# Kernel optimization log

Hardware: AMD Instinct MI355X
Metric: run time of the kernel (lower is better)

## Reference

```python
import jax, jax.numpy as jnp
import numpy as np
from jax import lax

EPS = 1e-12

def _l2norm(x):
    # F.normalize(x, dim=-1): x / max(||x||, eps)
    n = jnp.sqrt(jnp.sum(x * x, axis=-1, keepdims=True))
    return x / jnp.maximum(n, EPS)

def _knn_edges(z, k):
    """k nearest neighbors (excluding self) via squared euclidean distance.
    Squared distance preserves the top-k ordering of torch.cdist."""
    N = z.shape[0]
    sq = jnp.sum(z * z, axis=1)                        # [N]
    d2 = sq[:, None] + sq[None, :] - 2.0 * (z @ z.T)   # [N, N]
    _, idx = lax.top_k(-d2, k + 1)                     # nearest first; col 0 is self
    tgt = idx[:, 1:].reshape(-1)                       # [N*k]
    src = jnp.repeat(jnp.arange(N, dtype=idx.dtype), k)
    return src, tgt

def _count_components(A):
    """Connected components on dense boolean adjacency A [N,N] via
    min-label propagation with pointer jumping (jit-friendly BFS replacement)."""
    N = A.shape[0]
    labels0 = jnp.arange(N, dtype=jnp.int32)

    def cond(state):
        return state[1]

    def body(state):
        labels, _ = state
        # min label over neighbors (N as sentinel where no edge)
        nbr_min = jnp.min(jnp.where(A, labels[None, :], jnp.int32(N)), axis=1)
        new = jnp.minimum(labels, nbr_min)
        new = new[new]  # pointer jumping: label of my label
        return new, jnp.any(new != labels)

    labels, _ = lax.while_loop(cond, body, (labels0, jnp.array(True)))
    # a node whose final label equals its own index is the component minimum
    return jnp.sum(labels == jnp.arange(N, dtype=jnp.int32))

def _level(feats, W, ratio):
    N = feats.shape[0]
    z = _l2norm(feats @ W.T)                 # Linear(bias=False) then normalize
    k = max(3, int(ratio * N))               # static python int
    k = min(k, N - 1)
    src, tgt = _knn_edges(z, k)
    A = jnp.zeros((N, N), dtype=bool)
    A = A.at[src, tgt].set(True).at[tgt, src].set(True)   # symmetrize
    comps = _count_components(lax.stop_gradient(A))
    num_edges = N * k                                     # src.numel() in torch code
    b0 = comps
    b1 = jnp.maximum(0, num_edges - N + comps)
    return b0, b1

RATIOS = (0.1, 0.05)

def setup_inputs() -> dict:
    key = jax.random.key(0)
    k1, k2, k3 = jax.random.split(key, 3)
    N, C = 4096, 512
    feats = jax.random.normal(k1, (N, C), dtype=jnp.float32)
    W0 = jax.random.normal(k2, (512, C), dtype=jnp.float32) / np.sqrt(C)
    W1 = jax.random.normal(k3, (256, C), dtype=jnp.float32) / np.sqrt(C)
    return {"feats": feats, "W0": W0, "W1": W1}

def reference(feats, W0, W1):
    b0_0, b1_0 = _level(feats, W0, RATIOS[0])
    b0_1, b1_1 = _level(feats, W1, RATIOS[1])
    return jnp.stack([b0_0 + b0_1, b1_0 + b1_1]).astype(jnp.float32)
```

## Files before the change

### kernel.cpp

```cpp
#include <hip/hip_runtime.h>
#include <hip/hip_bf16.h>

#define NPTS   4096
#define ADJ_W  128

typedef __attribute__((ext_vector_type(8))) short short8;
typedef __attribute__((ext_vector_type(8))) unsigned short u16x8;
typedef __attribute__((ext_vector_type(4))) unsigned short u16x4;
typedef __attribute__((ext_vector_type(16))) unsigned char u8x16;
typedef __attribute__((ext_vector_type(4))) float f32x4;
typedef __attribute__((ext_vector_type(4))) int i32x4;
typedef __attribute__((ext_vector_type(4))) unsigned u32x4;

__device__ __forceinline__ unsigned short bf16_bits(float x) {
  __hip_bfloat16 h = __float2bfloat16(x);
  return __builtin_bit_cast(unsigned short, h);
}

__device__ __forceinline__ unsigned char quant8(float f) {
  return (unsigned char)(int)fminf(fmaxf((f + 0.25f) * 512.0f, 0.0f), 255.0f);
}

__device__ __forceinline__ void async16(const void* g, void* l) {
  __builtin_amdgcn_global_load_lds(
      (const __attribute__((address_space(1))) void*)g,
      (__attribute__((address_space(3))) void*)l, 16, 0, 0);
}

__global__ __launch_bounds__(256) void convert_all(
    const float* __restrict__ feats, const float* __restrict__ W0,
    const float* __restrict__ W1, unsigned short* __restrict__ fh,
    unsigned short* __restrict__ wcat) {
  const int NF = 4096 * 512 / 4, NW0 = 512 * 512 / 4, NW1 = 256 * 512 / 4;
  for (int u = blockIdx.x * 256 + threadIdx.x; u < NF + NW0 + NW1;
       u += gridDim.x * 256) {
    const float* src;
    unsigned short* dst;
    int idx;
    if (u < NF)            { src = feats; dst = fh;   idx = u; }
    else if (u < NF + NW0) { src = W0;    dst = wcat; idx = u - NF; }
    else                   { src = W1;    dst = wcat + NW0 * 4; idx = u - NF - NW0; }
    f32x4 v = *(const f32x4*)(src + (size_t)idx * 4);
    u16x4 o;
    #pragma unroll
    for (int e = 0; e < 4; e++) o[e] = bf16_bits(v[e]);
    *(u16x4*)(dst + (size_t)idx * 4) = o;
  }
}

__global__ __launch_bounds__(256) void gemm_bt_f32(
    const __hip_bfloat16* __restrict__ A, const __hip_bfloat16* __restrict__ B,
    float* __restrict__ C, int M, int N, int K) {
  __shared__ __attribute__((aligned(16))) __hip_bfloat16 As[2][128 * 32];
  __shared__ __attribute__((aligned(16))) __hip_bfloat16 Bs[2][128 * 32];
  int tid = threadIdx.x;
  int lane = tid & 63, wave = tid >> 6;
  int wr = wave >> 1, wc = wave & 1;
  int row0 = blockIdx.y * 128, col0 = blockIdx.x * 128;

  f32x4 acc[4][4] = {};
  int r = lane & 15, kh = lane >> 4;

  auto stage = [&](int buf, int k0) {
    #pragma unroll
    for (int q = 0; q < 2; q++) {
      int chunk = q * 256 + tid;
      int row = chunk >> 2;
      int cb = chunk & 3;
      async16(&A[(size_t)(row0 + row) * K + k0 + cb * 8],
              &As[buf][(q * 256 + wave * 64) * 8]);
      async16(&B[(size_t)(col0 + row) * K + k0 + cb * 8],
              &Bs[buf][(q * 256 + wave * 64) * 8]);
    }
  };

  int nt = K >> 5;
  stage(0, 0);
  int cur = 0;
  for (int t = 0; t < nt; t++) {
    if (t + 1 < nt) {
      stage(cur ^ 1, (t + 1) * 32);
      asm volatile("s_waitcnt vmcnt(4)" ::: "memory");
    } else {
      asm volatile("s_waitcnt vmcnt(0)" ::: "memory");
    }
    __builtin_amdgcn_s_barrier();
    __builtin_amdgcn_sched_barrier(0);

    short8 a[4], b[4];
    #pragma unroll
    for (int mi = 0; mi < 4; mi++)
      a[mi] = *(short8*)(&As[cur][(wr * 64 + mi * 16 + r) * 32 + kh * 8]);
    #pragma unroll
    for (int ni = 0; ni < 4; ni++)
      b[ni] = *(short8*)(&Bs[cur][(wc * 64 + ni * 16 + r) * 32 + kh * 8]);
    #pragma unroll
    for (int mi = 0; mi < 4; mi++)
      #pragma unroll
      for (int ni = 0; ni < 4; ni++)
        acc[mi][ni] = __builtin_amdgcn_mfma_f32_16x16x32_bf16(a[mi], b[ni], acc[mi][ni], 0, 0, 0);
    __builtin_amdgcn_s_barrier();
    cur ^= 1;
  }

  int rq = lane >> 4;
  #pragma unroll
  for (int mi = 0; mi < 4; mi++)
    #pragma unroll
    for (int ni = 0; ni < 4; ni++)
      #pragma unroll
      for (int j = 0; j < 4; j++) {
        int rr = row0 + wr * 64 + mi * 16 + rq * 4 + j;
        int cc = col0 + wc * 64 + ni * 16 + r;
        C[(size_t)rr * N + cc] = acc[mi][ni][j];
      }
}

__global__ __launch_bounds__(512) void gemm_s_tri(
    const __hip_bfloat16* __restrict__ Z0, const __hip_bfloat16* __restrict__ Z1,
    unsigned char* __restrict__ S0, unsigned char* __restrict__ S1) {
  __shared__ __attribute__((aligned(16))) __hip_bfloat16 As[3][128 * 32];
  __shared__ __attribute__((aligned(16))) __hip_bfloat16 Bs[3][128 * 32];
  unsigned char* Cs = (unsigned char*)As;

  int b = blockIdx.x;
  int s = (b & 7) * 132 + (b >> 3);
  int lvl = s & 1;
  int t = s >> 1;
  int I = (int)((sqrtf(8.0f * (float)t + 1.0f) - 1.0f) * 0.5f);
  if (t - I * (I + 1) / 2 > I) I++;
  int J = t - I * (I + 1) / 2;

  const __hip_bfloat16* Z = lvl ? Z1 : Z0;
  unsigned char* S = lvl ? S1 : S0;
  int K = lvl ? 256 : 512;
  int row0 = I * 128, col0 = J * 128;

  int tid = threadIdx.x;
  int lane = tid & 63, wave = tid >> 6;
  int wr = wave >> 2, wc = wave & 3;

  f32x4 acc[4][2] = {};
  int r = lane & 15, kh = lane >> 4, rq = lane >> 4;

  auto stage = [&](int buf, int k0) {
    int row = tid >> 2;
    int cb = tid & 3;
    async16(&Z[(size_t)(row0 + row) * K + k0 + cb * 8],
            &As[buf][(wave * 64) * 8]);
    async16(&Z[(size_t)(col0 + row) * K + k0 + cb * 8],
            &Bs[buf][(wave * 64) * 8]);
  };

  int nt = K >> 5;
  stage(0, 0);
  stage(1, 32);
  for (int tt = 0; tt < nt; tt++) {
    int cur = tt % 3;
    if (tt + 2 < nt) stage((tt + 2) % 3, (tt + 2) * 32);
    if (tt + 3 <= nt) {
      asm volatile("s_waitcnt vmcnt(4)" ::: "memory");
    } else if (tt + 2 == nt) {
      asm volatile("s_waitcnt vmcnt(2)" ::: "memory");
    } else {
      asm volatile("s_waitcnt vmcnt(0)" ::: "memory");
    }
    __builtin_amdgcn_s_barrier();
    __builtin_amdgcn_sched_barrier(0);

    short8 a[4], bfr[2];
    #pragma unroll
    for (int mi = 0; mi < 4; mi++)
      a[mi] = *(short8*)(&As[cur][(wr * 64 + mi * 16 + r) * 32 + kh * 8]);
    #pragma unroll
    for (int ni = 0; ni < 2; ni++)
      bfr[ni] = *(short8*)(&Bs[cur][(wc * 32 + ni * 16 + r) * 32 + kh * 8]);
    #pragma unroll
    for (int mi = 0; mi < 4; mi++)
      #pragma unroll
      for (int ni = 0; ni < 2; ni++)
        acc[mi][ni] = __builtin_amdgcn_mfma_f32_16x16x32_bf16(a[mi], bfr[ni], acc[mi][ni], 0, 0, 0);
    __builtin_amdgcn_s_barrier();
  }
  __syncthreads();

  int erow = tid >> 4;
  int ecol = (tid & 15) * 8;

  #pragma unroll
  for (int s4 = 0; s4 < 4; s4++) {
    if (wr == (s4 >> 1)) {
      const int half = s4 & 1;
      #pragma unroll
      for (int mi_l = 0; mi_l < 2; mi_l++) {
        const int mi = half * 2 + mi_l;
        #pragma unroll
        for (int ni = 0; ni < 2; ni++) {
          int lrow0 = mi * 16 + rq * 4 - half * 32;
          int cc = wc * 32 + ni * 16 + r;
          #pragma unroll
          for (int j = 0; j < 4; j++)
            Cs[(lrow0 + j) * 144 + cc] = quant8(acc[mi][ni][j]);
        }
      }
    }
    __syncthreads();
    {
      unsigned long long v = *(const unsigned long long*)(&Cs[erow * 144 + ecol]);
      *(unsigned long long*)(&S[(size_t)(row0 + s4 * 32 + erow) * NPTS + col0 + ecol]) = v;
    }
    __syncthreads();
  }

  if (I != J) {
    #pragma unroll
    for (int s4 = 0; s4 < 4; s4++) {
      if (wc == s4) {
        #pragma unroll
        for (int ni = 0; ni < 2; ni++) {
          int lrow = ni * 16 + r;
          #pragma unroll
          for (int mi = 0; mi < 4; mi++) {
            int rr = wr * 64 + mi * 16 + rq * 4;
            unsigned v = (unsigned)quant8(acc[mi][ni][0])
                       | ((unsigned)quant8(acc[mi][ni][1]) << 8)
                       | ((unsigned)quant8(acc[mi][ni][2]) << 16)
                       | ((unsigned)quant8(acc[mi][ni][3]) << 24);
            *(unsigned*)(&Cs[lrow * 144 + rr]) = v;
          }
        }
      }
      __syncthreads();
      {
        unsigned long long v = *(const unsigned long long*)(&Cs[erow * 144 + ecol]);
        *(unsigned long long*)(&S[(size_t)(col0 + s4 * 32 + erow) * NPTS + row0 + ecol]) = v;
      }
      __syncthreads();
    }
  }
}

__global__ __launch_bounds__(64) void l2norm_fused(const float* __restrict__ Zcat,
                                                   unsigned short* __restrict__ Z0h,
                                                   unsigned short* __restrict__ Z1h) {
  int bid = blockIdx.x;
  int lvl = bid >> 12, row = bid & 4095;
  int D = lvl ? 256 : 512;
  const float* src = Zcat + (size_t)row * 768 + (lvl ? 512 : 0);
  unsigned short* dst = lvl ? (Z1h + (size_t)row * 256) : (Z0h + (size_t)row * 512);
  int d4 = D >> 2;
  int lane = threadIdx.x;
  float ss = 0.f;
  for (int j = lane; j < d4; j += 64) {
    f32x4 v = *(const f32x4*)(src + j * 4);
    ss += v[0] * v[0] + v[1] * v[1] + v[2] * v[2] + v[3] * v[3];
  }
  #pragma unroll
  for (int off = 32; off; off >>= 1) ss += __shfl_xor(ss, off);
  float inv = 1.0f / fmaxf(sqrtf(ss), 1e-12f);
  for (int j = lane; j < d4; j += 64) {
    f32x4 v = *(const f32x4*)(src + j * 4);
    u16x4 o;
    #pragma unroll
    for (int e = 0; e < 4; e++) o[e] = bf16_bits(v[e] * inv);
    *(u16x4*)(dst + j * 4) = o;
  }
}

__global__ __launch_bounds__(256) void select_mark_f(
    const unsigned char* __restrict__ S0, const unsigned char* __restrict__ S1,
    unsigned* __restrict__ adjR) {
  __shared__ int hist[4][256];
  __shared__ int sfx[257];
  __shared__ int wtot[4];
  __shared__ unsigned rowbits[ADJ_W];
  __shared__ int sh_b;
  int bid = blockIdx.x;
  int lvl = bid >> 12, i = bid & 4095;
  int k = lvl ? 204 : 409;
  const unsigned char* row = (lvl ? S1 : S0) + (size_t)i * NPTS;
  unsigned* adj = adjR + ((size_t)lvl * NPTS + i) * ADJ_W;
  int tid = threadIdx.x;
  int lane = tid & 63, wid = tid >> 6;
  int target = k + 1;

  #pragma unroll
  for (int w = 0; w < 4; w++) hist[w][tid] = 0;
  if (tid < ADJ_W) rowbits[tid] = 0;
  __syncthreads();

  u8x16 v = *(const u8x16*)(row + tid * 16);
  #pragma unroll
  for (int e = 0; e < 16; e++)
    atomicAdd(&hist[wid][v[e]], 1);
  __syncthreads();

  {
    int c = hist[0][tid] + hist[1][tid] + hist[2][tid] + hist[3][tid];
    int sv = c;
    #pragma unroll
    for (int off = 1; off < 64; off <<= 1) {
      int u = __shfl_down(sv, off);
      if (lane + off < 64) sv += u;
    }
    if (lane == 0) wtot[wid] = sv;
    __syncthreads();
    int add = 0;
    for (int w = wid + 1; w < 4; w++) add += wtot[w];
    sfx[tid] = sv + add;
    if (tid == 0) sfx[256] = 0;
  }
  __syncthreads();
  if (sfx[tid] >= target && sfx[tid + 1] < target) sh_b = tid;
  __syncthreads();
  int bq = sh_b;

  #pragma unroll
  for (int e = 0; e < 16; e++) {
    int j = tid * 16 + e;
    if ((int)v[e] >= bq) atomicOr(&rowbits[j >> 5], 1u << (j & 31));
  }
  __syncthreads();
  if (tid == 0) rowbits[i >> 5] &= ~(1u << (i & 31));
  __syncthreads();
  if (tid < ADJ_W) adj[tid] = rowbits[tid];
}

__global__ __launch_bounds__(256) void sym_or_f(const unsigned* __restrict__ adjR,
                                                unsigned* __restrict__ adjS) {
  int bid = blockIdx.x;
  int lvl = bid >> 11;
  size_t base = (size_t)lvl * NPTS * ADJ_W;
  int tid = threadIdx.x;
  int lane = tid & 63, wave = tid >> 6;
  int half = lane >> 5, l = lane & 31;
  int tile = (bid & 2047) * 8 + wave * 2 + half;
  int I = tile >> 7, J = tile & 127;
  unsigned y = adjR[base + (size_t)(J * 32 + l) * ADJ_W + I];
  #pragma unroll
  for (int j = 16; j; j >>= 1) {
    unsigned m = 0xFFFFFFFFu / ((1u << j) + 1u);
    unsigned t = __shfl_xor(y, j);
    y = ((l & j) == 0) ? ((y & m) | ((t & m) << j))
                       : ((y & ~m) | ((t >> j) & m));
  }
  size_t d = base + (size_t)(I * 32 + l) * ADJ_W + J;
  adjS[d] = adjR[d] | y;
}

__global__ __launch_bounds__(256) void sweep0_f(const unsigned* __restrict__ adjS,
                                                int* __restrict__ labels) {
  int gi = blockIdx.x * 256 + threadIdx.x;
  int lvl = gi >> 12, node = gi & 4095;
  const unsigned* row = adjS + ((size_t)lvl * NPTS + node) * ADJ_W;
  int m = node;
  for (int w = 0; w < ADJ_W; w += 4) {
    u32x4 v = *(const u32x4*)(row + w);
    if (v[0]) { m = min(m, (w + 0) * 32 + __ffs(v[0]) - 1); break; }
    if (v[1]) { m = min(m, (w + 1) * 32 + __ffs(v[1]) - 1); break; }
    if (v[2]) { m = min(m, (w + 2) * 32 + __ffs(v[2]) - 1); break; }
    if (v[3]) { m = min(m, (w + 3) * 32 + __ffs(v[3]) - 1); break; }
  }
  labels[gi] = m;
}

__global__ __launch_bounds__(128) void prop_f(const unsigned* __restrict__ adjS,
                                              int* __restrict__ labels) {
  __shared__ int L[NPTS];
  int bid = blockIdx.x;
  int lvl = bid >> 12, i = bid & 4095;
  const unsigned* adj = adjS + ((size_t)lvl * NPTS + i) * ADJ_W;
  int* lab = labels + (lvl << 12);
  for (int t = threadIdx.x * 4; t < NPTS; t += 128 * 4)
    *(i32x4*)&L[t] = *(const i32x4*)&lab[t];
  __syncthreads();
  int w = threadIdx.x;
  unsigned bits = adj[w];
  int base = w << 5;
  int m = 0x7FFFFFFF;
  while (bits) {
    int b = __ffs(bits) - 1;
    bits &= bits - 1;
    m = min(m, L[base + b]);
  }
  #pragma unroll
  for (int off = 32; off; off >>= 1) m = min(m, __shfl_down(m, off));
  __shared__ int s2[2];
  if ((w & 63) == 0) s2[w >> 6] = m;
  __syncthreads();
  if (w == 0) {
    int mm = min(min(s2[0], s2[1]), L[i]);
    mm = min(mm, lab[mm]);
    lab[i] = mm;
  }
}

__global__ __launch_bounds__(256) void finalize2(const int* __restrict__ labels,
                                                 float* __restrict__ out) {
  __shared__ int c[2];
  int tid = threadIdx.x;
  if (tid < 2) c[tid] = 0;
  __syncthreads();
  int c0 = 0, c1 = 0;
  for (int j = tid; j < NPTS; j += 256) {
    c0 += (labels[j] == j);
    c1 += (labels[NPTS + j] == j);
  }
  #pragma unroll
  for (int off = 32; off; off >>= 1) {
    c0 += __shfl_down(c0, off);
    c1 += __shfl_down(c1, off);
  }
  if ((tid & 63) == 0) {
    atomicAdd(&c[0], c0);
    atomicAdd(&c[1], c1);
  }
  __syncthreads();
  if (tid == 0) {
    float f0 = (float)c[0], f1 = (float)c[1];
    float ne0 = 4096.f * 409.f, ne1 = 4096.f * 204.f;
    out[0] = f0 + f1;
    out[1] = fmaxf(0.f, ne0 - 4096.f + f0) + fmaxf(0.f, ne1 - 4096.f + f1);
  }
}

extern "C" void kernel_launch(void* const* d_in, const int* in_sizes, int n_in,
                              void* d_out, int out_size, void* d_ws, size_t ws_size,
                              hipStream_t stream) {
  const float* feats = (const float*)d_in[0];
  const float* W0    = (const float*)d_in[1];
  const float* W1    = (const float*)d_in[2];
  float* out = (float*)d_out;

  char* ws = (char*)d_ws;
  unsigned char*  S0      = (unsigned char*)(ws);
  unsigned char*  S1      = (unsigned char*)(ws + (16ull << 20));
  float*          Zcat    = (float*)(ws + (32ull << 20));
  __hip_bfloat16* Z0h     = (__hip_bfloat16*)(ws + (44ull << 20));
  __hip_bfloat16* Z1h     = (__hip_bfloat16*)(ws + (48ull << 20));
  __hip_bfloat16* fh      = (__hip_bfloat16*)(ws + (50ull << 20));
  __hip_bfloat16* wcat    = (__hip_bfloat16*)(ws + (54ull << 20));
  unsigned*       adjR    = (unsigned*)(ws + (55ull << 20));
  unsigned*       adjS    = (unsigned*)(ws + (59ull << 20));
  int*            labels  = (int*)(ws + (63ull << 20));

  convert_all<<<2048, 256, 0, stream>>>(feats, W0, W1,
                                        (unsigned short*)fh, (unsigned short*)wcat);
  gemm_bt_f32<<<dim3(768 / 128, 4096 / 128), 256, 0, stream>>>(
      fh, wcat, Zcat, 4096, 768, 512);
  l2norm_fused<<<8192, 64, 0, stream>>>(Zcat, (unsigned short*)Z0h,
                                        (unsigned short*)Z1h);
  gemm_s_tri<<<1056, 512, 0, stream>>>(Z0h, Z1h, S0, S1);
  select_mark_f<<<2 * NPTS, 256, 0, stream>>>(S0, S1, adjR);
  sym_or_f<<<4096, 256, 0, stream>>>(adjR, adjS);
  sweep0_f<<<32, 256, 0, stream>>>(adjS, labels);
  prop_f<<<2 * NPTS, 128, 0, stream>>>(adjS, labels);
  finalize2<<<1, 256, 0, stream>>>(labels, out);
}
```

Before: 111.8 us.

## Fuse L2 normalization into projection GEMM epilogue and defer scaling to similarity GEMM

The projection GEMM now writes unnormalized bf16 Z directly and accumulates row squared norms with atomics, replacing the fp32 Zcat buffer and the separate l2norm kernel. A tiny kernel turns the sums into inverse norms, which the similarity GEMM applies per row and column in its quantization epilogue. Tiles shrink from 128 to 64 to give the projection GEMM more blocks. This removes one fp32 round trip through memory. The cost is float atomics, which make the norms non-deterministic, and quantizing unnormalized bf16 values, which changes rounding slightly.

```diff
diff --git a/kernel.cpp b/kernel.cpp
--- a/kernel.cpp
+++ b/kernel.cpp
@@ -5,7 +5,6 @@
 #define ADJ_W  128
 
 typedef __attribute__((ext_vector_type(8))) short short8;
-typedef __attribute__((ext_vector_type(8))) unsigned short u16x8;
 typedef __attribute__((ext_vector_type(4))) unsigned short u16x4;
 typedef __attribute__((ext_vector_type(16))) unsigned char u8x16;
 typedef __attribute__((ext_vector_type(4))) float f32x4;
@@ -30,8 +29,10 @@
 __global__ __launch_bounds__(256) void convert_all(
     const float* __restrict__ feats, const float* __restrict__ W0,
     const float* __restrict__ W1, unsigned short* __restrict__ fh,
-    unsigned short* __restrict__ wcat) {
+    unsigned short* __restrict__ wcat, float* __restrict__ nsq) {
   const int NF = 4096 * 512 / 4, NW0 = 512 * 512 / 4, NW1 = 256 * 512 / 4;
+  for (int g = blockIdx.x * 256 + threadIdx.x; g < 2 * NPTS; g += gridDim.x * 256)
+    nsq[g] = 0.0f;
   for (int u = blockIdx.x * 256 + threadIdx.x; u < NF + NW0 + NW1;
        u += gridDim.x * 256) {
     const float* src;
@@ -48,79 +49,98 @@
   }
 }
 
-__global__ __launch_bounds__(256) void gemm_bt_f32(
-    const __hip_bfloat16* __restrict__ A, const __hip_bfloat16* __restrict__ B,
-    float* __restrict__ C, int M, int N, int K) {
-  __shared__ __attribute__((aligned(16))) __hip_bfloat16 As[2][128 * 32];
-  __shared__ __attribute__((aligned(16))) __hip_bfloat16 Bs[2][128 * 32];
+__global__ __launch_bounds__(256) void gemm_z_n(
+    const __hip_bfloat16* __restrict__ fh, const __hip_bfloat16* __restrict__ wcat,
+    unsigned short* __restrict__ Z0h, unsigned short* __restrict__ Z1h,
+    float* __restrict__ nsq) {
+  __shared__ __attribute__((aligned(16))) __hip_bfloat16 As[2][64 * 32];
+  __shared__ __attribute__((aligned(16))) __hip_bfloat16 Bs[2][64 * 32];
+  const int K = 512;
   int tid = threadIdx.x;
   int lane = tid & 63, wave = tid >> 6;
   int wr = wave >> 1, wc = wave & 1;
-  int row0 = blockIdx.y * 128, col0 = blockIdx.x * 128;
-
-  f32x4 acc[4][4] = {};
+  int row0 = blockIdx.y * 64, col0 = blockIdx.x * 64;
+
+  f32x4 acc[2][2] = {};
   int r = lane & 15, kh = lane >> 4;
 
   auto stage = [&](int buf, int k0) {
-    #pragma unroll
-    for (int q = 0; q < 2; q++) {
-      int chunk = q * 256 + tid;
-      int row = chunk >> 2;
-      int cb = chunk & 3;
-      async16(&A[(size_t)(row0 + row) * K + k0 + cb * 8],
-              &As[buf][(q * 256 + wave * 64) * 8]);
-      async16(&B[(size_t)(col0 + row) * K + k0 + cb * 8],
-              &Bs[buf][(q * 256 + wave * 64) * 8]);
-    }
+    int row = tid >> 2;
+    int cb = tid & 3;
+    async16(&fh[(size_t)(row0 + row) * K + k0 + cb * 8],
+            &As[buf][(wave * 64) * 8]);
+    async16(&wcat[(size_t)(col0 + row) * K + k0 + cb * 8],
+            &Bs[buf][(wave * 64) * 8]);
   };
 
-  int nt = K >> 5;
+  const int nt = K >> 5;
   stage(0, 0);
   int cur = 0;
   for (int t = 0; t < nt; t++) {
     if (t + 1 < nt) {
       stage(cur ^ 1, (t + 1) * 32);
-      asm volatile("s_waitcnt vmcnt(4)" ::: "memory");
+      asm volatile("s_waitcnt vmcnt(2)" ::: "memory");
     } else {
       asm volatile("s_waitcnt vmcnt(0)" ::: "memory");
     }
     __builtin_amdgcn_s_barrier();
     __builtin_amdgcn_sched_barrier(0);
 
-    short8 a[4], b[4];
-    #pragma unroll
-    for (int mi = 0; mi < 4; mi++)
-      a[mi] = *(short8*)(&As[cur][(wr * 64 + mi * 16 + r) * 32 + kh * 8]);
-    #pragma unroll
-    for (int ni = 0; ni < 4; ni++)
-      b[ni] = *(short8*)(&Bs[cur][(wc * 64 + ni * 16 + r) * 32 + kh * 8]);
-    #pragma unroll
-    for (int mi = 0; mi < 4; mi++)
-      #pragma unroll
-      for (int ni = 0; ni < 4; ni++)
+    short8 a[2], b[2];
+    #pragma unroll
+    for (int mi = 0; mi < 2; mi++)
+      a[mi] = *(short8*)(&As[cur][(wr * 32 + mi * 16 + r) * 32 + kh * 8]);
+    #pragma unroll
+    for (int ni = 0; ni < 2; ni++)
+      b[ni] = *(short8*)(&Bs[cur][(wc * 32 + ni * 16 + r) * 32 + kh * 8]);
+    #pragma unroll
+    for (int mi = 0; mi < 2; mi++)
+      #pragma unroll
+      for (int ni = 0; ni < 2; ni++)
         acc[mi][ni] = __builtin_amdgcn_mfma_f32_16x16x32_bf16(a[mi], b[ni], acc[mi][ni], 0, 0, 0);
     __builtin_amdgcn_s_barrier();
     cur ^= 1;
   }
 
   int rq = lane >> 4;
-  #pragma unroll
-  for (int mi = 0; mi < 4; mi++)
-    #pragma unroll
-    for (int ni = 0; ni < 4; ni++)
-      #pragma unroll
-      for (int j = 0; j < 4; j++) {
-        int rr = row0 + wr * 64 + mi * 16 + rq * 4 + j;
-        int cc = col0 + wc * 64 + ni * 16 + r;
-        C[(size_t)rr * N + cc] = acc[mi][ni][j];
+  int lvl = (col0 >= 512);
+  unsigned short* Zh = lvl ? Z1h : Z0h;
+  int cbase = (lvl ? col0 - 512 : col0) + wc * 32;
+  int D = lvl ? 256 : 512;
+  float* nq = nsq + (lvl << 12);
+
+  #pragma unroll
+  for (int mi = 0; mi < 2; mi++)
+    #pragma unroll
+    for (int j = 0; j < 4; j++) {
+      int rr = row0 + wr * 32 + mi * 16 + rq * 4 + j;
+      float ss = 0.f;
+      #pragma unroll
+      for (int ni = 0; ni < 2; ni++) {
+        float v = acc[mi][ni][j];
+        ss += v * v;
       }
+      #pragma unroll
+      for (int off = 1; off < 16; off <<= 1) ss += __shfl_xor(ss, off);
+      if (r == 0) atomicAdd(&nq[rr], ss);
+      #pragma unroll
+      for (int ni = 0; ni < 2; ni++)
+        Zh[(size_t)rr * D + cbase + ni * 16 + r] = bf16_bits(acc[mi][ni][j]);
+    }
+}
+
+__global__ __launch_bounds__(256) void inv_norms(float* __restrict__ nsq) {
+  int g = blockIdx.x * 256 + threadIdx.x;
+  if (g < 2 * NPTS) nsq[g] = 1.0f / fmaxf(sqrtf(nsq[g]), 1e-12f);
 }
 
 __global__ __launch_bounds__(512) void gemm_s_tri(
     const __hip_bfloat16* __restrict__ Z0, const __hip_bfloat16* __restrict__ Z1,
-    unsigned char* __restrict__ S0, unsigned char* __restrict__ S1) {
+    unsigned char* __restrict__ S0, unsigned char* __restrict__ S1,
+    const float* __restrict__ invn) {
   __shared__ __attribute__((aligned(16))) __hip_bfloat16 As[3][128 * 32];
   __shared__ __attribute__((aligned(16))) __hip_bfloat16 Bs[3][128 * 32];
+  __shared__ float invRs[128], invCs[128];
   unsigned char* Cs = (unsigned char*)As;
 
   int b = blockIdx.x;
@@ -182,6 +202,11 @@
         acc[mi][ni] = __builtin_amdgcn_mfma_f32_16x16x32_bf16(a[mi], bfr[ni], acc[mi][ni], 0, 0, 0);
     __builtin_amdgcn_s_barrier();
   }
+  {
+    const float* nl = invn + (lvl << 12);
+    if (tid < 128)            invRs[tid] = nl[row0 + tid];
+    else if (tid < 256)       invCs[tid - 128] = nl[col0 + tid - 128];
+  }
   __syncthreads();
 
   int erow = tid >> 4;
@@ -198,9 +223,11 @@
         for (int ni = 0; ni < 2; ni++) {
           int lrow0 = mi * 16 + rq * 4 - half * 32;
           int cc = wc * 32 + ni * 16 + r;
+          float sc_c = invCs[cc];
           #pragma unroll
           for (int j = 0; j < 4; j++)
-            Cs[(lrow0 + j) * 144 + cc] = quant8(acc[mi][ni][j]);
+            Cs[(lrow0 + j) * 144 + cc] =
+                quant8(acc[mi][ni][j] * invRs[wr * 64 + mi * 16 + rq * 4 + j] * sc_c);
         }
       }
     }
@@ -219,13 +246,15 @@
         #pragma unroll
         for (int ni = 0; ni < 2; ni++) {
           int lrow = ni * 16 + r;
+          float sc_c = invCs[wc * 32 + ni * 16 + r];
           #pragma unroll
           for (int mi = 0; mi < 4; mi++) {
             int rr = wr * 64 + mi * 16 + rq * 4;
-            unsigned v = (unsigned)quant8(acc[mi][ni][0])
-                       | ((unsigned)quant8(acc[mi][ni][1]) << 8)
-                       | ((unsigned)quant8(acc[mi][ni][2]) << 16)
-                       | ((unsigned)quant8(acc[mi][ni][3]) << 24);
+            unsigned v =
+                  (unsigned)quant8(acc[mi][ni][0] * invRs[rr + 0] * sc_c)
+                | ((unsigned)quant8(acc[mi][ni][1] * invRs[rr + 1] * sc_c) << 8)
+                | ((unsigned)quant8(acc[mi][ni][2] * invRs[rr + 2] * sc_c) << 16)
+                | ((unsigned)quant8(acc[mi][ni][3] * invRs[rr + 3] * sc_c) << 24);
             *(unsigned*)(&Cs[lrow * 144 + rr]) = v;
           }
         }
@@ -237,33 +266,6 @@
       }
       __syncthreads();
     }
-  }
-}
-
-__global__ __launch_bounds__(64) void l2norm_fused(const float* __restrict__ Zcat,
-                                                   unsigned short* __restrict__ Z0h,
-                                                   unsigned short* __restrict__ Z1h) {
-  int bid = blockIdx.x;
-  int lvl = bid >> 12, row = bid & 4095;
-  int D = lvl ? 256 : 512;
-  const float* src = Zcat + (size_t)row * 768 + (lvl ? 512 : 0);
-  unsigned short* dst = lvl ? (Z1h + (size_t)row * 256) : (Z0h + (size_t)row * 512);
-  int d4 = D >> 2;
-  int lane = threadIdx.x;
-  float ss = 0.f;
-  for (int j = lane; j < d4; j += 64) {
-    f32x4 v = *(const f32x4*)(src + j * 4);
-    ss += v[0] * v[0] + v[1] * v[1] + v[2] * v[2] + v[3] * v[3];
-  }
-  #pragma unroll
-  for (int off = 32; off; off >>= 1) ss += __shfl_xor(ss, off);
-  float inv = 1.0f / fmaxf(sqrtf(ss), 1e-12f);
-  for (int j = lane; j < d4; j += 64) {
-    f32x4 v = *(const f32x4*)(src + j * 4);
-    u16x4 o;
-    #pragma unroll
-    for (int e = 0; e < 4; e++) o[e] = bf16_bits(v[e] * inv);
-    *(u16x4*)(dst + j * 4) = o;
   }
 }
 
@@ -435,22 +437,22 @@
   char* ws = (char*)d_ws;
   unsigned char*  S0      = (unsigned char*)(ws);
   unsigned char*  S1      = (unsigned char*)(ws + (16ull << 20));
-  float*          Zcat    = (float*)(ws + (32ull << 20));
-  __hip_bfloat16* Z0h     = (__hip_bfloat16*)(ws + (44ull << 20));
-  __hip_bfloat16* Z1h     = (__hip_bfloat16*)(ws + (48ull << 20));
-  __hip_bfloat16* fh      = (__hip_bfloat16*)(ws + (50ull << 20));
-  __hip_bfloat16* wcat    = (__hip_bfloat16*)(ws + (54ull << 20));
-  unsigned*       adjR    = (unsigned*)(ws + (55ull << 20));
-  unsigned*       adjS    = (unsigned*)(ws + (59ull << 20));
-  int*            labels  = (int*)(ws + (63ull << 20));
+  __hip_bfloat16* Z0h     = (__hip_bfloat16*)(ws + (32ull << 20));
+  __hip_bfloat16* Z1h     = (__hip_bfloat16*)(ws + (36ull << 20));
+  __hip_bfloat16* fh      = (__hip_bfloat16*)(ws + (38ull << 20));
+  __hip_bfloat16* wcat    = (__hip_bfloat16*)(ws + (42ull << 20));
+  float*          invn    = (float*)(ws + (43ull << 20));
+  unsigned*       adjR    = (unsigned*)(ws + (44ull << 20));
+  unsigned*       adjS    = (unsigned*)(ws + (48ull << 20));
+  int*            labels  = (int*)(ws + (52ull << 20));
 
   convert_all<<<2048, 256, 0, stream>>>(feats, W0, W1,
-                                        (unsigned short*)fh, (unsigned short*)wcat);
-  gemm_bt_f32<<<dim3(768 / 128, 4096 / 128), 256, 0, stream>>>(
-      fh, wcat, Zcat, 4096, 768, 512);
-  l2norm_fused<<<8192, 64, 0, stream>>>(Zcat, (unsigned short*)Z0h,
-                                        (unsigned short*)Z1h);
-  gemm_s_tri<<<1056, 512, 0, stream>>>(Z0h, Z1h, S0, S1);
+                                        (unsigned short*)fh, (unsigned short*)wcat,
+                                        invn);
+  gemm_z_n<<<dim3(768 / 64, 4096 / 64), 256, 0, stream>>>(
+      fh, wcat, (unsigned short*)Z0h, (unsigned short*)Z1h, invn);
+  inv_norms<<<32, 256, 0, stream>>>(invn);
+  gemm_s_tri<<<1056, 512, 0, stream>>>(Z0h, Z1h, S0, S1, invn);
   select_mark_f<<<2 * NPTS, 256, 0, stream>>>(S0, S1, adjR);
   sym_or_f<<<4096, 256, 0, stream>>>(adjR, adjS);
   sweep0_f<<<32, 256, 0, stream>>>(adjS, labels);
```

Measured after the change: 109.9 us. No clear change (-1.8%).
